# Performance work log

Hardware: AMD Instinct MI355X
Metric: run time of the kernel (lower is better)

Reference implementation:

```python
import jax, jax.numpy as jnp
import numpy as np

B = 1024            # batch
F = (16, 16, 16)    # factors (f1, f2, f3)
BOND = 32           # bond dimension
SIZE = 4096         # prod(F)


def setup_inputs() -> dict:
    key = jax.random.key(0)
    k0, k1, k2, k3 = jax.random.split(key, 4)
    x = jax.random.normal(k0, (B, SIZE), dtype=jnp.float32)
    # cores: (r_{k-1}, f_k, f_k, r_k), boundary ranks = 1, init scale 0.01 as in torch
    core0 = jax.random.normal(k1, (1, F[0], F[0], BOND), dtype=jnp.float32) * 0.01
    core1 = jax.random.normal(k2, (BOND, F[1], F[1], BOND), dtype=jnp.float32) * 0.01
    core2 = jax.random.normal(k3, (BOND, F[2], F[2], 1), dtype=jnp.float32) * 0.01
    bias = jnp.zeros((SIZE,), dtype=jnp.float32)
    return {"x": x, "core0": core0, "core1": core1, "core2": core2, "bias": bias}


def reference(x, core0, core1, core2, bias):
    # Batched MPO (tensor-train) matvec: y[b, i1 i2 i3] = sum_{j1 j2 j3, r1 r2}
    #   G0[1, i1, j1, r1] G1[r1, i2, j2, r2] G2[r2, i3, j3, 1] * x[b, j1 j2 j3]
    b = x.shape[0]
    t = x.reshape(b, F[0], F[1], F[2])                       # (B, j1, j2, j3)
    # contract j1 with core0 -> carry bond r, accumulate output index i1 at the end
    t = jnp.einsum('bjkl,aijr->brkli', t, core0)             # (B, r1, j2, j3, i1)
    # contract (r1, j2) with core1
    t = jnp.einsum('brkli,rmks->bslim', t, core1)            # (B, r2, j3, i1, i2)
    # contract (r2, j3) with core2 (right bond t has size 1)
    y = jnp.einsum('bslim,snlt->bimnt', t, core2)            # (B, i1, i2, i3, 1)
    return y.reshape(b, SIZE) + bias
```

## Files before the change

kernel.cpp:

```cpp
#include <hip/hip_runtime.h>
#include <stdint.h>

typedef float f32x4_t __attribute__((ext_vector_type(4)));
typedef __bf16 bf16x8_t __attribute__((ext_vector_type(8)));

#define GLD16(gp, lp) __builtin_amdgcn_global_load_lds( \
    (const __attribute__((address_space(1))) void*)(gp), \
    (__attribute__((address_space(3))) void*)(lp), 16, 0, 0)

__device__ __forceinline__ uint32_t f2bf(float f) {
  uint32_t u = __float_as_uint(f);
  u += 0x7FFFu + ((u >> 16) & 1u);
  return u >> 16;
}
__device__ __forceinline__ uint32_t pack2(float a, float b) {
  return f2bf(a) | (f2bf(b) << 16);
}

__global__ __launch_bounds__(256) void build_m01_kernel(
    const float* __restrict__ c0, const float* __restrict__ c1,
    float* __restrict__ M01) {
  const int a = blockIdx.x, t = threadIdx.x;
  const int i1 = a >> 4, i2 = a & 15, j1 = t >> 4, j2 = t & 15;
  const float* c0p = c0 + (i1 * 16 + j1) * 32;
  const float4* c1v = (const float4*)(c1 + i2 * 512 + j2 * 32);

  float acc[32];
  #pragma unroll
  for (int r2 = 0; r2 < 32; ++r2) acc[r2] = 0.f;

  #pragma unroll 4
  for (int r1 = 0; r1 < 32; ++r1) {
    const float g = c0p[r1];
    #pragma unroll
    for (int q = 0; q < 8; ++q) {
      const float4 v = c1v[r1 * 2048 + q];
      acc[q * 4 + 0] += g * v.x; acc[q * 4 + 1] += g * v.y;
      acc[q * 4 + 2] += g * v.z; acc[q * 4 + 3] += g * v.w;
    }
  }
  float4* dst = (float4*)(M01 + (size_t)a * 8192 + t * 32);
  #pragma unroll
  for (int q = 0; q < 8; ++q) {
    float4 v = {acc[q * 4 + 0], acc[q * 4 + 1], acc[q * 4 + 2], acc[q * 4 + 3]};
    dst[q] = v;
  }
}

__global__ __launch_bounds__(256) void build_w2_kernel(
    const float* __restrict__ M01, const float* __restrict__ c2,
    uint16_t* __restrict__ W) {
  __shared__ float C2L[4][512];
  const int bid0 = blockIdx.x;
  const int bid = (bid0 & 7) * 128 + (bid0 >> 3);
  const int a = bid >> 2, i3q = (bid & 3) << 2;
  const int t = threadIdx.x;

  #pragma unroll
  for (int s = 0; s < 2; ++s) {
    const int idx = t * 2 + s;
    const int sl = idx >> 7;
    const int rem = idx & 127;
    ((float4*)C2L[sl])[rem] =
        ((const float4*)c2)[(rem >> 2) * 64 + (i3q + sl) * 4 + (rem & 3)];
  }
  __syncthreads();

  float M[32];
  const float4* mp = (const float4*)(M01 + (size_t)a * 8192 + t * 32);
  #pragma unroll
  for (int q = 0; q < 8; ++q) {
    const float4 v = mp[q];
    M[q * 4 + 0] = v.x; M[q * 4 + 1] = v.y; M[q * 4 + 2] = v.z; M[q * 4 + 3] = v.w;
  }

  #pragma unroll 1
  for (int i3l = 0; i3l < 4; ++i3l) {
    float acc[16];
    #pragma unroll
    for (int j = 0; j < 16; ++j) acc[j] = 0.f;

    const float* C2s = C2L[i3l];
    #pragma unroll 4
    for (int r2 = 0; r2 < 32; ++r2) {
      const float4* cp = (const float4*)(C2s + r2 * 16);
      const float4 q0 = cp[0], q1 = cp[1], q2 = cp[2], q3 = cp[3];
      const float m = M[r2];
      acc[0]  += m * q0.x; acc[1]  += m * q0.y; acc[2]  += m * q0.z; acc[3]  += m * q0.w;
      acc[4]  += m * q1.x; acc[5]  += m * q1.y; acc[6]  += m * q1.z; acc[7]  += m * q1.w;
      acc[8]  += m * q2.x; acc[9]  += m * q2.y; acc[10] += m * q2.z; acc[11] += m * q2.w;
      acc[12] += m * q3.x; acc[13] += m * q3.y; acc[14] += m * q3.z; acc[15] += m * q3.w;
    }

    uint4 o0, o1;
    o0.x = pack2(acc[0],  acc[1]);  o0.y = pack2(acc[2],  acc[3]);
    o0.z = pack2(acc[4],  acc[5]);  o0.w = pack2(acc[6],  acc[7]);
    o1.x = pack2(acc[8],  acc[9]);  o1.y = pack2(acc[10], acc[11]);
    o1.z = pack2(acc[12], acc[13]); o1.w = pack2(acc[14], acc[15]);
    uint4* dst = (uint4*)(W + (size_t)(a * 16 + i3q + i3l) * 4096 + t * 16);
    dst[0] = o0; dst[1] = o1;
  }
}

__global__ __launch_bounds__(256) void cvt_x_kernel(const float* __restrict__ x,
                                                    uint32_t* __restrict__ xb) {
  const int i = blockIdx.x * 256 + threadIdx.x;
  const float4* x4 = (const float4*)x;
  const float4 a = x4[2 * i], b = x4[2 * i + 1];
  uint4 o;
  o.x = pack2(a.x, a.y); o.y = pack2(a.z, a.w);
  o.z = pack2(b.x, b.y); o.w = pack2(b.z, b.w);
  ((uint4*)xb)[i] = o;
}

__global__ __launch_bounds__(256, 2) void gemm_bt_bias_kernel(
    const uint16_t* __restrict__ A, const uint16_t* __restrict__ Bt,
    const float* __restrict__ bias, float* __restrict__ C) {
  constexpr int Kd = 4096, Nd = 4096;
  __shared__ uint16_t As[64 * 64];
  __shared__ uint16_t Bs[128 * 64];
  const int t = threadIdx.x;
  const int wid = t >> 6, lane = t & 63;

  const int bid = blockIdx.x;
  const int g = bid & 7, idx = bid >> 3;
  const int ntile = g * 4 + (idx >> 4);
  const int mtile = idx & 15;
  const int brow = mtile * 64, bcol = ntile * 128;

  const uint16_t* Ab = A + (size_t)brow * Kd;
  const uint16_t* Bb = Bt + (size_t)bcol * Kd;

  const int rb = t >> 3;
  const int ce = ((t & 7) * 8) ^ ((rb & 7) << 3);
  const uint16_t* gA = Ab + (size_t)rb * Kd + ce;
  const uint16_t* gB = Bb + (size_t)rb * Kd + ce;
  uint16_t* lA0 = As + wid * 512;
  uint16_t* lA1 = As + 2048 + wid * 512;
  uint16_t* lB0 = Bs + wid * 512;
  uint16_t* lB1 = Bs + 2048 + wid * 512;
  uint16_t* lB2 = Bs + 4096 + wid * 512;
  uint16_t* lB3 = Bs + 6144 + wid * 512;

  const int wm = wid >> 1, wn = wid & 1;
  const int fr = lane & 15, fk = (lane >> 4) * 8;
  const int csw = (fr & 7) << 3;

  f32x4_t zero = {0.f, 0.f, 0.f, 0.f};
  f32x4_t acc[2][4];
  #pragma unroll
  for (int m = 0; m < 2; ++m)
    #pragma unroll
    for (int n = 0; n < 4; ++n) acc[m][n] = zero;

  for (int kt = 0; kt < Kd; kt += 64) {
    GLD16(gA + kt, lA0);
    GLD16(gA + (size_t)32 * Kd + kt, lA1);
    GLD16(gB + kt, lB0);
    GLD16(gB + (size_t)32 * Kd + kt, lB1);
    GLD16(gB + (size_t)64 * Kd + kt, lB2);
    GLD16(gB + (size_t)96 * Kd + kt, lB3);
    __syncthreads();

    bf16x8_t af[2][2], bfr[2][4];
    #pragma unroll
    for (int kk = 0; kk < 2; ++kk) {
      const int col = (kk * 32 + fk) ^ csw;
      #pragma unroll
      for (int m = 0; m < 2; ++m)
        af[kk][m] = *(const bf16x8_t*)(As + (wm * 32 + m * 16 + fr) * 64 + col);
      #pragma unroll
      for (int n = 0; n < 4; ++n)
        bfr[kk][n] = *(const bf16x8_t*)(Bs + (wn * 64 + n * 16 + fr) * 64 + col);
    }
    #pragma unroll
    for (int kk = 0; kk < 2; ++kk)
      #pragma unroll
      for (int m = 0; m < 2; ++m)
        #pragma unroll
        for (int n = 0; n < 4; ++n)
          acc[m][n] = __builtin_amdgcn_mfma_f32_16x16x32_bf16(
              af[kk][m], bfr[kk][n], acc[m][n], 0, 0, 0);
    __syncthreads();
  }

  const int orow = brow + wm * 32 + (lane >> 4) * 4;
  const int ocol = bcol + wn * 64 + fr;
  #pragma unroll
  for (int n = 0; n < 4; ++n) {
    const float bv = bias[ocol + n * 16];
    #pragma unroll
    for (int m = 0; m < 2; ++m) {
      float* Cp = C + (size_t)(orow + m * 16) * Nd + ocol + n * 16;
      #pragma unroll
      for (int r = 0; r < 4; ++r) Cp[(size_t)r * Nd] = acc[m][n][r] + bv;
    }
  }
}

extern "C" void kernel_launch(void* const* d_in, const int* in_sizes, int n_in,
                              void* d_out, int out_size, void* d_ws, size_t ws_size,
                              hipStream_t stream) {
  const float* x    = (const float*)d_in[0];
  const float* c0   = (const float*)d_in[1];
  const float* c1   = (const float*)d_in[2];
  const float* c2   = (const float*)d_in[3];
  const float* bias = (const float*)d_in[4];
  float* y = (float*)d_out;

  uint16_t* W    = (uint16_t*)d_ws;
  char*     slab = (char*)d_ws + (size_t)4096 * 4096 * 2;
  float*    M01  = (float*)slab;
  uint16_t* xb   = (uint16_t*)slab;

  build_m01_kernel<<<256, 256, 0, stream>>>(c0, c1, M01);
  build_w2_kernel<<<1024, 256, 0, stream>>>(M01, c2, W);
  cvt_x_kernel<<<2048, 256, 0, stream>>>(x, (uint32_t*)xb);
  gemm_bt_bias_kernel<<<512, 256, 0, stream>>>(xb, W, bias, y);
}
```

Baseline: 182.4 us.

## Double-buffer GEMM LDS tiles and enlarge block tile to 128x128

The GEMM block tile grows from 64x128 to 128x128, so each wave computes a 64x64 sub-tile with 16 accumulators and the grid halves to 256 blocks. Shared-memory tiles are double-buffered so the next K-slice's global-to-LDS loads are issued before the current slice's MFMAs, removing one barrier per iteration. The r2 loop in build_w2 is fully unrolled. The intent is more reuse per LDS load and overlap of loads with compute, at the cost of more registers and LDS, occupancy lowered to one block per SIMD set, and only 256 blocks to spread across the CUs.

After: 216.2 us. 1.19x slower.

```diff
diff --git a/kernel.cpp b/kernel.cpp
--- a/kernel.cpp
+++ b/kernel.cpp
@@ -81,7 +81,7 @@
     for (int j = 0; j < 16; ++j) acc[j] = 0.f;
 
     const float* C2s = C2L[i3l];
-    #pragma unroll 4
+    #pragma unroll
     for (int r2 = 0; r2 < 32; ++r2) {
       const float4* cp = (const float4*)(C2s + r2 * 16);
       const float4 q0 = cp[0], q1 = cp[1], q2 = cp[2], q3 = cp[3];
@@ -113,84 +113,86 @@
   ((uint4*)xb)[i] = o;
 }
 
-__global__ __launch_bounds__(256, 2) void gemm_bt_bias_kernel(
+__global__ __launch_bounds__(256, 1) void gemm_bt_bias_kernel(
     const uint16_t* __restrict__ A, const uint16_t* __restrict__ Bt,
     const float* __restrict__ bias, float* __restrict__ C) {
   constexpr int Kd = 4096, Nd = 4096;
-  __shared__ uint16_t As[64 * 64];
-  __shared__ uint16_t Bs[128 * 64];
+  __shared__ uint16_t As[2][128 * 64];
+  __shared__ uint16_t Bs[2][128 * 64];
   const int t = threadIdx.x;
   const int wid = t >> 6, lane = t & 63;
 
   const int bid = blockIdx.x;
   const int g = bid & 7, idx = bid >> 3;
-  const int ntile = g * 4 + (idx >> 4);
-  const int mtile = idx & 15;
-  const int brow = mtile * 64, bcol = ntile * 128;
-
-  const uint16_t* Ab = A + (size_t)brow * Kd;
-  const uint16_t* Bb = Bt + (size_t)bcol * Kd;
+  const int ntile = g * 4 + (idx >> 3);
+  const int mtile = idx & 7;
+  const int brow = mtile * 128, bcol = ntile * 128;
 
   const int rb = t >> 3;
   const int ce = ((t & 7) * 8) ^ ((rb & 7) << 3);
-  const uint16_t* gA = Ab + (size_t)rb * Kd + ce;
-  const uint16_t* gB = Bb + (size_t)rb * Kd + ce;
-  uint16_t* lA0 = As + wid * 512;
-  uint16_t* lA1 = As + 2048 + wid * 512;
-  uint16_t* lB0 = Bs + wid * 512;
-  uint16_t* lB1 = Bs + 2048 + wid * 512;
-  uint16_t* lB2 = Bs + 4096 + wid * 512;
-  uint16_t* lB3 = Bs + 6144 + wid * 512;
+  const uint16_t* gA = A + (size_t)(brow + rb) * Kd + ce;
+  const uint16_t* gB = Bt + (size_t)(bcol + rb) * Kd + ce;
+  const int wofs = wid * 512;
 
   const int wm = wid >> 1, wn = wid & 1;
   const int fr = lane & 15, fk = (lane >> 4) * 8;
   const int csw = (fr & 7) << 3;
 
   f32x4_t zero = {0.f, 0.f, 0.f, 0.f};
-  f32x4_t acc[2][4];
-  #pragma unroll
-  for (int m = 0; m < 2; ++m)
+  f32x4_t acc[4][4];
+  #pragma unroll
+  for (int m = 0; m < 4; ++m)
     #pragma unroll
     for (int n = 0; n < 4; ++n) acc[m][n] = zero;
 
+  #define STAGE(buf, kt)                                                      \
+    do {                                                                      \
+      _Pragma("unroll")                                                       \
+      for (int i = 0; i < 4; ++i) {                                           \
+        GLD16(gA + (size_t)i * 32 * Kd + (kt), As[buf] + i * 2048 + wofs);    \
+        GLD16(gB + (size_t)i * 32 * Kd + (kt), Bs[buf] + i * 2048 + wofs);    \
+      }                                                                       \
+    } while (0)
+
+  STAGE(0, 0);
+  __syncthreads();
+
+  int cur = 0;
   for (int kt = 0; kt < Kd; kt += 64) {
-    GLD16(gA + kt, lA0);
-    GLD16(gA + (size_t)32 * Kd + kt, lA1);
-    GLD16(gB + kt, lB0);
-    GLD16(gB + (size_t)32 * Kd + kt, lB1);
-    GLD16(gB + (size_t)64 * Kd + kt, lB2);
-    GLD16(gB + (size_t)96 * Kd + kt, lB3);
-    __syncthreads();
-
-    bf16x8_t af[2][2], bfr[2][4];
+    if (kt + 64 < Kd) STAGE(cur ^ 1, kt + 64);
+
+    bf16x8_t af[2][4], bfr[2][4];
     #pragma unroll
     for (int kk = 0; kk < 2; ++kk) {
       const int col = (kk * 32 + fk) ^ csw;
       #pragma unroll
-      for (int m = 0; m < 2; ++m)
-        af[kk][m] = *(const bf16x8_t*)(As + (wm * 32 + m * 16 + fr) * 64 + col);
+      for (int m = 0; m < 4; ++m)
+        af[kk][m] = *(const bf16x8_t*)(As[cur] + (wm * 64 + m * 16 + fr) * 64 + col);
       #pragma unroll
       for (int n = 0; n < 4; ++n)
-        bfr[kk][n] = *(const bf16x8_t*)(Bs + (wn * 64 + n * 16 + fr) * 64 + col);
+        bfr[kk][n] = *(const bf16x8_t*)(Bs[cur] + (wn * 64 + n * 16 + fr) * 64 + col);
     }
     #pragma unroll
     for (int kk = 0; kk < 2; ++kk)
       #pragma unroll
-      for (int m = 0; m < 2; ++m)
+      for (int m = 0; m < 4; ++m)
         #pragma unroll
         for (int n = 0; n < 4; ++n)
           acc[m][n] = __builtin_amdgcn_mfma_f32_16x16x32_bf16(
               af[kk][m], bfr[kk][n], acc[m][n], 0, 0, 0);
+
     __syncthreads();
-  }
-
-  const int orow = brow + wm * 32 + (lane >> 4) * 4;
+    cur ^= 1;
+  }
+  #undef STAGE
+
+  const int orow = brow + wm * 64 + (lane >> 4) * 4;
   const int ocol = bcol + wn * 64 + fr;
   #pragma unroll
   for (int n = 0; n < 4; ++n) {
     const float bv = bias[ocol + n * 16];
     #pragma unroll
-    for (int m = 0; m < 2; ++m) {
+    for (int m = 0; m < 4; ++m) {
       float* Cp = C + (size_t)(orow + m * 16) * Nd + ocol + n * 16;
       #pragma unroll
       for (int r = 0; r < 4; ++r) Cp[(size_t)r * Nd] = acc[m][n][r] + bv;
@@ -216,5 +218,5 @@
   build_m01_kernel<<<256, 256, 0, stream>>>(c0, c1, M01);
   build_w2_kernel<<<1024, 256, 0, stream>>>(M01, c2, W);
   cvt_x_kernel<<<2048, 256, 0, stream>>>(x, (uint32_t*)xb);
-  gemm_bt_bias_kernel<<<512, 256, 0, stream>>>(xb, W, bias, y);
-}
+  gemm_bt_bias_kernel<<<256, 256, 0, stream>>>(xb, W, bias, y);
+}
```

## Use split-K double-buffered 128x128 GEMM with separate bias reduction

Applied to the files above, without the earlier changes.

Replaces the 64x128-tile GEMM with a 128x128-tile, split-K-by-two kernel that double-buffers LDS loads so the next K slice is fetched while MFMAs run. The two partial results go to the output and a workspace slab, and a separate reduce kernel sums them and adds the bias. The goal is more data reuse per tile and overlap of loads with compute, at the cost of an extra kernel launch and an extra fp32 write and read of the full output. It also fully unrolls the r2 loop in build_w2, and keeps the old path as a fallback when the workspace is too small.

Result: slower. 196.2 us (+7.5%).

```diff
diff --git a/kernel.cpp b/kernel.cpp
--- a/kernel.cpp
+++ b/kernel.cpp
@@ -81,7 +81,7 @@
     for (int j = 0; j < 16; ++j) acc[j] = 0.f;
 
     const float* C2s = C2L[i3l];
-    #pragma unroll 4
+    #pragma unroll
     for (int r2 = 0; r2 < 32; ++r2) {
       const float4* cp = (const float4*)(C2s + r2 * 16);
       const float4 q0 = cp[0], q1 = cp[1], q2 = cp[2], q3 = cp[3];
@@ -113,6 +113,106 @@
   ((uint4*)xb)[i] = o;
 }
 
+__global__ __launch_bounds__(256, 2) void gemm_splitk_kernel(
+    const uint16_t* __restrict__ A, const uint16_t* __restrict__ Bt,
+    float* __restrict__ P0, float* __restrict__ P1) {
+  constexpr int Kd = 4096, Nd = 4096;
+  __shared__ uint16_t As[2][128 * 64];
+  __shared__ uint16_t Bs[2][128 * 64];
+  const int t = threadIdx.x;
+  const int wid = t >> 6, lane = t & 63;
+
+  const int bid = blockIdx.x;
+  const int g = bid & 7, idx = bid >> 3;
+  const int ntile = g * 4 + (idx >> 4);
+  const int mtile = (idx >> 1) & 7;
+  const int ks = idx & 1;
+  const int brow = mtile * 128, bcol = ntile * 128;
+  const int kbase = ks * 2048;
+
+  const int rb = t >> 3;
+  const int ce = ((t & 7) * 8) ^ ((rb & 7) << 3);
+  const uint16_t* gA = A + (size_t)(brow + rb) * Kd + kbase + ce;
+  const uint16_t* gB = Bt + (size_t)(bcol + rb) * Kd + kbase + ce;
+  const int wofs = wid * 512;
+
+  const int wm = wid >> 1, wn = wid & 1;
+  const int fr = lane & 15, fk = (lane >> 4) * 8;
+  const int csw = (fr & 7) << 3;
+
+  f32x4_t zero = {0.f, 0.f, 0.f, 0.f};
+  f32x4_t acc[4][4];
+  #pragma unroll
+  for (int m = 0; m < 4; ++m)
+    #pragma unroll
+    for (int n = 0; n < 4; ++n) acc[m][n] = zero;
+
+  #define STAGE(buf, kt)                                                      \
+    do {                                                                      \
+      _Pragma("unroll")                                                       \
+      for (int i = 0; i < 4; ++i) {                                           \
+        GLD16(gA + (size_t)i * 32 * Kd + (kt), As[buf] + i * 2048 + wofs);    \
+        GLD16(gB + (size_t)i * 32 * Kd + (kt), Bs[buf] + i * 2048 + wofs);    \
+      }                                                                       \
+    } while (0)
+
+  STAGE(0, 0);
+  __syncthreads();
+
+  int cur = 0;
+  for (int kt = 0; kt < 2048; kt += 64) {
+    if (kt + 64 < 2048) STAGE(cur ^ 1, kt + 64);
+
+    bf16x8_t af[2][4], bfr[2][4];
+    #pragma unroll
+    for (int kk = 0; kk < 2; ++kk) {
+      const int col = (kk * 32 + fk) ^ csw;
+      #pragma unroll
+      for (int m = 0; m < 4; ++m)
+        af[kk][m] = *(const bf16x8_t*)(As[cur] + (wm * 64 + m * 16 + fr) * 64 + col);
+      #pragma unroll
+      for (int n = 0; n < 4; ++n)
+        bfr[kk][n] = *(const bf16x8_t*)(Bs[cur] + (wn * 64 + n * 16 + fr) * 64 + col);
+    }
+    #pragma unroll
+    for (int kk = 0; kk < 2; ++kk)
+      #pragma unroll
+      for (int m = 0; m < 4; ++m)
+        #pragma unroll
+        for (int n = 0; n < 4; ++n)
+          acc[m][n] = __builtin_amdgcn_mfma_f32_16x16x32_bf16(
+              af[kk][m], bfr[kk][n], acc[m][n], 0, 0, 0);
+
+    __syncthreads();
+    cur ^= 1;
+  }
+  #undef STAGE
+
+  float* P = ks ? P1 : P0;
+  const int orow = brow + wm * 64 + (lane >> 4) * 4;
+  const int ocol = bcol + wn * 64 + fr;
+  #pragma unroll
+  for (int n = 0; n < 4; ++n) {
+    #pragma unroll
+    for (int m = 0; m < 4; ++m) {
+      float* Cp = P + (size_t)(orow + m * 16) * Nd + ocol + n * 16;
+      #pragma unroll
+      for (int r = 0; r < 4; ++r) Cp[(size_t)r * Nd] = acc[m][n][r];
+    }
+  }
+}
+
+__global__ __launch_bounds__(256) void reduce_kernel(
+    float* __restrict__ y, const float* __restrict__ p1,
+    const float* __restrict__ bias) {
+  const int i4 = blockIdx.x * 256 + threadIdx.x;
+  const float4 a = ((const float4*)y)[i4];
+  const float4 b = ((const float4*)p1)[i4];
+  const float4 c = ((const float4*)bias)[i4 & 1023];
+  float4 o = {a.x + b.x + c.x, a.y + b.y + c.y, a.z + b.z + c.z, a.w + b.w + c.w};
+  ((float4*)y)[i4] = o;
+}
+
 __global__ __launch_bounds__(256, 2) void gemm_bt_bias_kernel(
     const uint16_t* __restrict__ A, const uint16_t* __restrict__ Bt,
     const float* __restrict__ bias, float* __restrict__ C) {
@@ -121,16 +221,13 @@
   __shared__ uint16_t Bs[128 * 64];
   const int t = threadIdx.x;
   const int wid = t >> 6, lane = t & 63;
-
   const int bid = blockIdx.x;
   const int g = bid & 7, idx = bid >> 3;
   const int ntile = g * 4 + (idx >> 4);
   const int mtile = idx & 15;
   const int brow = mtile * 64, bcol = ntile * 128;
-
   const uint16_t* Ab = A + (size_t)brow * Kd;
   const uint16_t* Bb = Bt + (size_t)bcol * Kd;
-
   const int rb = t >> 3;
   const int ce = ((t & 7) * 8) ^ ((rb & 7) << 3);
   const uint16_t* gA = Ab + (size_t)rb * Kd + ce;
@@ -141,18 +238,15 @@
   uint16_t* lB1 = Bs + 2048 + wid * 512;
   uint16_t* lB2 = Bs + 4096 + wid * 512;
   uint16_t* lB3 = Bs + 6144 + wid * 512;
-
   const int wm = wid >> 1, wn = wid & 1;
   const int fr = lane & 15, fk = (lane >> 4) * 8;
   const int csw = (fr & 7) << 3;
-
   f32x4_t zero = {0.f, 0.f, 0.f, 0.f};
   f32x4_t acc[2][4];
   #pragma unroll
   for (int m = 0; m < 2; ++m)
     #pragma unroll
     for (int n = 0; n < 4; ++n) acc[m][n] = zero;
-
   for (int kt = 0; kt < Kd; kt += 64) {
     GLD16(gA + kt, lA0);
     GLD16(gA + (size_t)32 * Kd + kt, lA1);
@@ -161,7 +255,6 @@
     GLD16(gB + (size_t)64 * Kd + kt, lB2);
     GLD16(gB + (size_t)96 * Kd + kt, lB3);
     __syncthreads();
-
     bf16x8_t af[2][2], bfr[2][4];
     #pragma unroll
     for (int kk = 0; kk < 2; ++kk) {
@@ -183,7 +276,6 @@
               af[kk][m], bfr[kk][n], acc[m][n], 0, 0, 0);
     __syncthreads();
   }
-
   const int orow = brow + wm * 32 + (lane >> 4) * 4;
   const int ocol = bcol + wn * 64 + fr;
   #pragma unroll
@@ -212,9 +304,17 @@
   char*     slab = (char*)d_ws + (size_t)4096 * 4096 * 2;
   float*    M01  = (float*)slab;
   uint16_t* xb   = (uint16_t*)slab;
+  float*    P1   = (float*)((char*)d_ws + (size_t)40 * 1024 * 1024);
+  const size_t need = (size_t)40 * 1024 * 1024 + (size_t)1024 * 4096 * 4;
 
   build_m01_kernel<<<256, 256, 0, stream>>>(c0, c1, M01);
   build_w2_kernel<<<1024, 256, 0, stream>>>(M01, c2, W);
   cvt_x_kernel<<<2048, 256, 0, stream>>>(x, (uint32_t*)xb);
-  gemm_bt_bias_kernel<<<512, 256, 0, stream>>>(xb, W, bias, y);
-}
+
+  if (ws_size >= need) {
+    gemm_splitk_kernel<<<512, 256, 0, stream>>>(xb, W, y, P1);
+    reduce_kernel<<<4096, 256, 0, stream>>>(y, P1, bias);
+  } else {
+    gemm_bt_bias_kernel<<<512, 256, 0, stream>>>(xb, W, bias, y);
+  }
+}
```
